# Optimization experiments

Hardware: AMD Instinct MI355X
Metric: run time of the kernel (lower is better)

## Reference

```python
import jax, jax.numpy as jnp
import numpy as np

D_HEAD = 128


def setup_inputs() -> dict:
    key = jax.random.key(0)
    k1, k2, k3 = jax.random.split(key, 3)
    batch, num_q, seq_len, d = 16, 64, 4096, D_HEAD
    query = jax.random.normal(k1, (batch, num_q, d), dtype=jnp.float32)
    keys = jax.random.normal(k2, (batch, seq_len, d), dtype=jnp.float32)
    values = jax.random.normal(k3, (batch, seq_len, d), dtype=jnp.float32)
    return {"query": query, "keys": keys, "values": values}


def reference(query, keys, values):
    # AttentionJacobian.forward with 3D query -> compute_attention_jacobian_batched
    # J[b,q] = scale * ( sum_n a[b,q,n] v[b,n] k[b,n]^T  -  (a V)[b,q] ((a K)[b,q])^T )
    d_k = keys.shape[-1]
    scale = d_k ** (-0.5)
    scores = jnp.einsum('bqd,bnd->bqn', query, keys) * scale
    attn_weights = jax.nn.softmax(scores, axis=-1)            # (b, q, n)
    attn_outputs = jnp.einsum('bqn,bnv->bqv', attn_weights, values)
    # term1 without materializing (b, q, n, v, k): fuse as single contraction
    term1 = jnp.einsum('bqn,bnv,bnk->bqvk', attn_weights, values, keys)
    weighted_keys_sum = jnp.einsum('bqn,bnk->bqk', attn_weights, keys)
    term2 = jnp.einsum('bqv,bqk->bqvk', attn_outputs, weighted_keys_sum)
    jacobians = scale * (term1 - term2)                       # (b, q, d_v, d_k)
    return jacobians
```

## Files before the change

### kernel.cpp

```cpp
#include <hip/hip_runtime.h>
#include <stdint.h>

typedef _Float16 f16;
typedef _Float16 half8 __attribute__((ext_vector_type(8)));
typedef float f32x4 __attribute__((ext_vector_type(4)));

#define BATCH 16
#define NQ 64
#define SL 4096
#define DH 128


__global__ __launch_bounds__(256) void kprep(const float* __restrict__ Kg,
                                             const float* __restrict__ Vg,
                                             f16* __restrict__ Kt,
                                             f16* __restrict__ Vt) {
  __shared__ f16 Ld[128][130];
  const int blk = blockIdx.x;
  const int b = blk >> 6;
  const int tensor = (blk >> 5) & 1;
  const int chunk = blk & 31;
  const float* src = tensor ? Vg : Kg;
  f16* dst = tensor ? Vt : Kt;
  const int t = threadIdx.x;
  const int n0 = chunk * 128;
  {
    const int d = t & 127;
    const int nl = t >> 7;
    const float* s = src + ((size_t)b * SL + n0 + nl) * DH + d;
    for (int it = 0; it < 64; ++it)
      Ld[d][nl + it * 2] = (f16)s[(size_t)it * 2 * DH];
  }
  __syncthreads();
  {
    const int r = t & 15;
    const int kc = (t >> 4) & 3;
    const int w = t >> 6;
    char* dstb = (char*)(dst + (size_t)b * DH * SL);
#pragma unroll
    for (int tl = 0; tl < 4; ++tl)
#pragma unroll
      for (int hh = 0; hh < 2; ++hh) {
        const int dhi = w + hh * 4;
        const int d = dhi * 16 + r;
        const int nl = tl * 32 + kc * 8;
        const half8 v = *(const half8*)&Ld[d][nl];
        *(half8*)(dstb + (size_t)(chunk * 4 + tl) * 8192 + dhi * 1024 +
                  kc * 256 + r * 16) = v;
      }
  }
}

__global__ __launch_bounds__(256) void kscore(const float* __restrict__ Q,
                                              const f16* __restrict__ Kt,
                                              f16* __restrict__ E) {
  const int blk = (blockIdx.x & 7) * 64 + (blockIdx.x >> 3);
  __shared__ float Qs[8][128];
  const int b = blk >> 5;
  const int qg = (blk >> 2) & 7;
  const int ns = blk & 3;
  const int t = threadIdx.x;
  for (int i = t; i < 8 * 128; i += 256)
    Qs[i >> 7][i & 127] = Q[((size_t)b * NQ + qg * 8 + (i >> 7)) * DH + (i & 127)];
  __syncthreads();
  const int w = t >> 6, l = t & 63;
  const int q0 = (w >> 1) * 4;
  const int nbase = ns * 1024 + (w & 1) * 512 + l * 8;
  const f16* kb = Kt + (size_t)b * DH * SL + (size_t)(nbase >> 5) * 4096 +
                  (size_t)((nbase >> 3) & 3) * 128;
  float acc[4][8] = {};
  for (int d = 0; d < DH; ++d) {
    const half8 kv = *(const half8*)(kb + (d >> 4) * 512 + (d & 15) * 8);
    float kf[8];
#pragma unroll
    for (int j = 0; j < 8; ++j) kf[j] = (float)kv[j];
#pragma unroll
    for (int qi = 0; qi < 4; ++qi) {
      const float qv = Qs[q0 + qi][d];
#pragma unroll
      for (int j = 0; j < 8; ++j) acc[qi][j] += qv * kf[j];
    }
  }
  const float scl = 0.08838834764831845f;
#pragma unroll
  for (int qi = 0; qi < 4; ++qi) {
    half8 ev;
#pragma unroll
    for (int j = 0; j < 8; ++j) ev[j] = (f16)__expf(acc[qi][j] * scl);
    *(half8*)&E[((size_t)b * NQ + qg * 8 + q0 + qi) * SL + nbase] = ev;
  }
}

__global__ __launch_bounds__(256) void kreduce(const f16* __restrict__ E,
                                               float* __restrict__ denom) {
  const int gw = blockIdx.x * 4 + (threadIdx.x >> 6);
  const int lane = threadIdx.x & 63;
  const f16* e = E + (size_t)gw * SL;
  float s = 0.f;
#pragma unroll
  for (int i = 0; i < 8; ++i) {
    const half8 h = *(const half8*)(e + i * 512 + lane * 8);
#pragma unroll
    for (int j = 0; j < 8; ++j) s += (float)h[j];
  }
  for (int off = 1; off < 64; off <<= 1) s += __shfl_xor(s, off);
  if (lane == 0) denom[gw] = s;
}

__global__ __launch_bounds__(256) void kev(const f16* __restrict__ Vt,
                                           const f16* __restrict__ Kt,
                                           const f16* __restrict__ E,
                                           float* __restrict__ EVp,
                                           float* __restrict__ EKp) {
  const int blk = (blockIdx.x & 7) * 32 + (blockIdx.x >> 3);
  const int b = blk >> 4;
  const int tensor = (blk >> 3) & 1;
  const int qq = (blk >> 1) & 3;
  const int nh = blk & 1;
  const char* src = (const char*)((tensor ? Kt : Vt) + (size_t)b * DH * SL);
  float* dst = (tensor ? EKp : EVp) +
               ((size_t)nh * BATCH * NQ + (size_t)b * NQ + qq * 16) * DH;
  const f16* Eb = E + ((size_t)b * NQ + qq * 16) * SL;
  const int t = threadIdx.x, w = t >> 6, l = t & 63;
  f32x4 acc[2] = {};
  for (int n0 = nh * 2048; n0 < nh * 2048 + 2048; n0 += 32) {
    const half8 a0 =
        *(const half8*)(src + (size_t)(n0 >> 5) * 8192 + w * 1024 + l * 16);
    const half8 a1 =
        *(const half8*)(src + (size_t)(n0 >> 5) * 8192 + (w + 4) * 1024 + l * 16);
    const half8 b0 =
        *(const half8*)(Eb + (size_t)(l & 15) * SL + n0 + (l >> 4) * 8);
    acc[0] = __builtin_amdgcn_mfma_f32_16x16x32_f16(a0, b0, acc[0], 0, 0, 0);
    acc[1] = __builtin_amdgcn_mfma_f32_16x16x32_f16(a1, b0, acc[1], 0, 0, 0);
  }
#pragma unroll
  for (int sv2 = 0; sv2 < 2; ++sv2) {
    const int q = l & 15;
    const int row = (w + sv2 * 4) * 16 + (l >> 4) * 4;
    *(f32x4*)&dst[(size_t)q * DH + row] = acc[sv2];
  }
}

__global__ __launch_bounds__(256, 2) void kjac(
    const f16* __restrict__ Vt, const f16* __restrict__ Kt,
    const f16* __restrict__ E, const float* __restrict__ EV,
    const float* __restrict__ EK, const float* __restrict__ denom,
    float* __restrict__ out) {
  const int blk = (blockIdx.x & 7) * 64 + (blockIdx.x >> 3);
  const int b = blk >> 5;
  const int q0 = (blk & 31) * 2;
  const int t = threadIdx.x, w = t >> 6, l = t & 63;
  const int sA = (w >> 1) * 4;
  const int sB = (w & 1) * 4;
  const char* vtb = (const char*)(Vt + (size_t)b * DH * SL) + sA * 1024 + l * 16;
  const char* ktb = (const char*)(Kt + (size_t)b * DH * SL) + sB * 1024 + l * 16;
  const f16* Eb = E + ((size_t)b * NQ + q0) * SL + (l >> 4) * 8;

  f32x4 acc[2][4][4] = {};
  half8 vfA[4], kfA[4], efA[2], vfB[4], kfB[4], efB[2];

#define LOADF(vf, kf, ef, tile)                                              \
  {                                                                          \
    const size_t gb = (size_t)(tile) * 8192;                                 \
    _Pragma("unroll") for (int i = 0; i < 4; ++i) vf[i] =                    \
        *(const half8*)(vtb + gb + i * 1024);                                \
    _Pragma("unroll") for (int j = 0; j < 4; ++j) kf[j] =                    \
        *(const half8*)(ktb + gb + j * 1024);                                \
    ef[0] = *(const half8*)(Eb + (tile) * 32);                               \
    ef[1] = *(const half8*)(Eb + SL + (tile) * 32);                          \
  }

#define MFMA32(vf, kf, ef)                                                   \
  {                                                                          \
    __builtin_amdgcn_s_setprio(1);                                           \
    _Pragma("unroll") for (int i = 0; i < 4; ++i) {                          \
      const half8 u0 = ef[0] * vf[i];                                        \
      const half8 u1 = ef[1] * vf[i];                                        \
      _Pragma("unroll") for (int j = 0; j < 4; ++j) {                        \
        acc[0][i][j] = __builtin_amdgcn_mfma_f32_16x16x32_f16(               \
            u0, kf[j], acc[0][i][j], 0, 0, 0);                               \
        acc[1][i][j] = __builtin_amdgcn_mfma_f32_16x16x32_f16(               \
            u1, kf[j], acc[1][i][j], 0, 0, 0);                               \
      }                                                                      \
    }                                                                        \
    __builtin_amdgcn_s_setprio(0);                                           \
  }

  LOADF(vfA, kfA, efA, 0)
  for (int tt = 0; tt < 126; tt += 2) {
    LOADF(vfB, kfB, efB, tt + 1)
    MFMA32(vfA, kfA, efA)
    LOADF(vfA, kfA, efA, tt + 2)
    MFMA32(vfB, kfB, efB)
  }
  LOADF(vfB, kfB, efB, 127)
  MFMA32(vfA, kfA, efA)
  MFMA32(vfB, kfB, efB)
#undef LOADF
#undef MFMA32

  const float scl = 0.08838834764831845f;
#pragma unroll
  for (int q = 0; q < 2; ++q) {
    const float invd = 1.0f / denom[b * NQ + q0 + q];
    const float* evq = EV + ((size_t)b * NQ + q0 + q) * DH;
    const float* evq2 = evq + (size_t)BATCH * NQ * DH;
    const float* ekq = EK + ((size_t)b * NQ + q0 + q) * DH;
    const float* ekq2 = ekq + (size_t)BATCH * NQ * DH;
    float* ob = out + (size_t)(b * NQ + q0 + q) * DH * DH;
#pragma unroll
    for (int i = 0; i < 4; ++i) {
      const int row0 = (sA + i) * 16 + (l >> 4) * 4;
      const f32x4 ev4 = *(const f32x4*)&evq[row0] + *(const f32x4*)&evq2[row0];
#pragma unroll
      for (int j = 0; j < 4; ++j) {
        const int col = (sB + j) * 16 + (l & 15);
        const float ek = ekq[col] + ekq2[col];
#pragma unroll
        for (int r = 0; r < 4; ++r)
          ob[(size_t)(row0 + r) * DH + col] =
              scl * invd * (acc[q][i][j][r] - invd * ev4[r] * ek);
      }
    }
  }
}

extern "C" void kernel_launch(void* const* d_in, const int* in_sizes, int n_in,
                              void* d_out, int out_size, void* d_ws,
                              size_t ws_size, hipStream_t stream) {
  const float* Q = (const float*)d_in[0];
  const float* K = (const float*)d_in[1];
  const float* V = (const float*)d_in[2];
  float* out = (float*)d_out;

  f16* Vt = (f16*)d_ws;
  f16* Kt = Vt + (size_t)BATCH * DH * SL;
  f16* Ef = Kt + (size_t)BATCH * DH * SL;
  float* EV = (float*)(Ef + (size_t)BATCH * NQ * SL);
  float* EK = EV + 2 * (size_t)BATCH * NQ * DH;
  float* denom = EK + 2 * (size_t)BATCH * NQ * DH;

  kprep<<<1024, 256, 0, stream>>>(K, V, Kt, Vt);
  kscore<<<512, 256, 0, stream>>>(Q, Kt, Ef);
  kreduce<<<256, 256, 0, stream>>>(Ef, denom);
  kev<<<256, 256, 0, stream>>>(Vt, Kt, Ef, EV, EK);
  kjac<<<512, 256, 0, stream>>>(Vt, Kt, Ef, EV, EK, denom, out);
}
```

Baseline: 185.9 us.

## Switch to 32x32x16 MFMA with matching fragment-ordered K/V layout

Changes the pre-swizzled K/V fp16 layout to match 32x32x16 MFMA operand fragments and rewrites kjac and kev to use 32x32 MFMA tiles instead of 16x16. Larger MFMA tiles raise arithmetic intensity per operand load and cut the number of MFMA issues and element-wise E*V multiplies per tile. kev is restructured to 128 blocks each covering 32 queries. This adds larger accumulator register pressure, and the epilogue stores become scalar rather than vectorised.

```diff
diff --git a/kernel.cpp b/kernel.cpp
--- a/kernel.cpp
+++ b/kernel.cpp
@@ -4,6 +4,7 @@
 typedef _Float16 f16;
 typedef _Float16 half8 __attribute__((ext_vector_type(8)));
 typedef float f32x4 __attribute__((ext_vector_type(4)));
+typedef float f32x16 __attribute__((ext_vector_type(16)));
 
 #define BATCH 16
 #define NQ 64
@@ -33,21 +34,17 @@
   }
   __syncthreads();
   {
-    const int r = t & 15;
-    const int kc = (t >> 4) & 3;
-    const int w = t >> 6;
-    char* dstb = (char*)(dst + (size_t)b * DH * SL);
-#pragma unroll
-    for (int tl = 0; tl < 4; ++tl)
-#pragma unroll
-      for (int hh = 0; hh < 2; ++hh) {
-        const int dhi = w + hh * 4;
-        const int d = dhi * 16 + r;
-        const int nl = tl * 32 + kc * 8;
-        const half8 v = *(const half8*)&Ld[d][nl];
-        *(half8*)(dstb + (size_t)(chunk * 4 + tl) * 8192 + dhi * 1024 +
-                  kc * 256 + r * 16) = v;
-      }
+    const int dblk = t >> 6;
+    const int khalf = (t >> 5) & 1;
+    const int r5 = t & 31;
+    const int d = dblk * 32 + r5;
+    f16* db = dst + (size_t)b * DH * SL;
+#pragma unroll
+    for (int ngl = 0; ngl < 8; ++ngl) {
+      const int nl = ngl * 16 + khalf * 8;
+      *(half8*)(db + (size_t)(chunk * 8 + ngl) * 2048 + dblk * 512 +
+                khalf * 256 + r5 * 8) = *(const half8*)&Ld[d][nl];
+    }
   }
 }
 
@@ -66,11 +63,11 @@
   const int w = t >> 6, l = t & 63;
   const int q0 = (w >> 1) * 4;
   const int nbase = ns * 1024 + (w & 1) * 512 + l * 8;
-  const f16* kb = Kt + (size_t)b * DH * SL + (size_t)(nbase >> 5) * 4096 +
-                  (size_t)((nbase >> 3) & 3) * 128;
+  const f16* kb = Kt + (size_t)b * DH * SL + (size_t)(nbase >> 4) * 2048 +
+                  (size_t)((nbase >> 3) & 1) * 256;
   float acc[4][8] = {};
   for (int d = 0; d < DH; ++d) {
-    const half8 kv = *(const half8*)(kb + (d >> 4) * 512 + (d & 15) * 8);
+    const half8 kv = *(const half8*)(kb + (d >> 5) * 512 + (d & 31) * 8);
     float kf[8];
 #pragma unroll
     for (int j = 0; j < 8; ++j) kf[j] = (float)kv[j];
@@ -112,32 +109,27 @@
                                            const f16* __restrict__ E,
                                            float* __restrict__ EVp,
                                            float* __restrict__ EKp) {
-  const int blk = (blockIdx.x & 7) * 32 + (blockIdx.x >> 3);
-  const int b = blk >> 4;
-  const int tensor = (blk >> 3) & 1;
-  const int qq = (blk >> 1) & 3;
-  const int nh = blk & 1;
+  const int blk = (blockIdx.x & 7) * 16 + (blockIdx.x >> 3);
+  const int b = blk >> 3;
+  const int tensor = (blk >> 2) & 1;
+  const int nh = (blk >> 1) & 1;
+  const int qh = blk & 1;
   const char* src = (const char*)((tensor ? Kt : Vt) + (size_t)b * DH * SL);
-  float* dst = (tensor ? EKp : EVp) +
-               ((size_t)nh * BATCH * NQ + (size_t)b * NQ + qq * 16) * DH;
-  const f16* Eb = E + ((size_t)b * NQ + qq * 16) * SL;
+  float* dst = (tensor ? EKp : EVp) + ((size_t)nh * BATCH * NQ + (size_t)b * NQ) * DH;
+  const f16* Eb = E + ((size_t)b * NQ + qh * 32) * SL;
   const int t = threadIdx.x, w = t >> 6, l = t & 63;
-  f32x4 acc[2] = {};
-  for (int n0 = nh * 2048; n0 < nh * 2048 + 2048; n0 += 32) {
-    const half8 a0 =
-        *(const half8*)(src + (size_t)(n0 >> 5) * 8192 + w * 1024 + l * 16);
-    const half8 a1 =
-        *(const half8*)(src + (size_t)(n0 >> 5) * 8192 + (w + 4) * 1024 + l * 16);
-    const half8 b0 =
-        *(const half8*)(Eb + (size_t)(l & 15) * SL + n0 + (l >> 4) * 8);
-    acc[0] = __builtin_amdgcn_mfma_f32_16x16x32_f16(a0, b0, acc[0], 0, 0, 0);
-    acc[1] = __builtin_amdgcn_mfma_f32_16x16x32_f16(a1, b0, acc[1], 0, 0, 0);
-  }
-#pragma unroll
-  for (int sv2 = 0; sv2 < 2; ++sv2) {
-    const int q = l & 15;
-    const int row = (w + sv2 * 4) * 16 + (l >> 4) * 4;
-    *(f32x4*)&dst[(size_t)q * DH + row] = acc[sv2];
+  f32x16 acc = {};
+  for (int ng = nh * 128; ng < nh * 128 + 128; ++ng) {
+    const half8 a = *(const half8*)(src + (size_t)ng * 4096 + w * 1024 + l * 16);
+    const half8 bb =
+        *(const half8*)(Eb + (size_t)(l & 31) * SL + ng * 16 + (l >> 5) * 8);
+    acc = __builtin_amdgcn_mfma_f32_32x32x16_f16(a, bb, acc, 0, 0, 0);
+  }
+  const int q = qh * 32 + (l & 31);
+#pragma unroll
+  for (int reg = 0; reg < 16; ++reg) {
+    const int row = w * 32 + (reg & 3) + 8 * (reg >> 2) + 4 * (l >> 5);
+    dst[(size_t)q * DH + row] = acc[reg];
   }
 }
 
@@ -150,37 +142,44 @@
   const int b = blk >> 5;
   const int q0 = (blk & 31) * 2;
   const int t = threadIdx.x, w = t >> 6, l = t & 63;
-  const int sA = (w >> 1) * 4;
-  const int sB = (w & 1) * 4;
-  const char* vtb = (const char*)(Vt + (size_t)b * DH * SL) + sA * 1024 + l * 16;
-  const char* ktb = (const char*)(Kt + (size_t)b * DH * SL) + sB * 1024 + l * 16;
-  const f16* Eb = E + ((size_t)b * NQ + q0) * SL + (l >> 4) * 8;
-
-  f32x4 acc[2][4][4] = {};
-  half8 vfA[4], kfA[4], efA[2], vfB[4], kfB[4], efB[2];
+  const int Mb = (w >> 1) * 64;
+  const int Nb = (w & 1) * 64;
+  const char* vtb =
+      (const char*)(Vt + (size_t)b * DH * SL) + (Mb >> 5) * 1024 + l * 16;
+  const char* ktb =
+      (const char*)(Kt + (size_t)b * DH * SL) + (Nb >> 5) * 1024 + l * 16;
+  const f16* Eb = E + ((size_t)b * NQ + q0) * SL + (l >> 5) * 8;
+
+  f32x16 acc[2][2][2] = {};
+  half8 vfA[2][2], kfA[2][2], efA[2][2];
+  half8 vfB[2][2], kfB[2][2], efB[2][2];
 
 #define LOADF(vf, kf, ef, tile)                                              \
   {                                                                          \
     const size_t gb = (size_t)(tile) * 8192;                                 \
-    _Pragma("unroll") for (int i = 0; i < 4; ++i) vf[i] =                    \
-        *(const half8*)(vtb + gb + i * 1024);                                \
-    _Pragma("unroll") for (int j = 0; j < 4; ++j) kf[j] =                    \
-        *(const half8*)(ktb + gb + j * 1024);                                \
-    ef[0] = *(const half8*)(Eb + (tile) * 32);                               \
-    ef[1] = *(const half8*)(Eb + SL + (tile) * 32);                          \
-  }
-
-#define MFMA32(vf, kf, ef)                                                   \
+    _Pragma("unroll") for (int s = 0; s < 2; ++s) {                          \
+      _Pragma("unroll") for (int di = 0; di < 2; ++di) vf[di][s] =           \
+          *(const half8*)(vtb + gb + s * 4096 + di * 1024);                  \
+      _Pragma("unroll") for (int dj = 0; dj < 2; ++dj) kf[dj][s] =           \
+          *(const half8*)(ktb + gb + s * 4096 + dj * 1024);                  \
+      _Pragma("unroll") for (int q = 0; q < 2; ++q) ef[q][s] =               \
+          *(const half8*)(Eb + q * SL + (tile) * 32 + s * 16);               \
+    }                                                                        \
+  }
+
+#define MFMA16(vf, kf, ef)                                                   \
   {                                                                          \
     __builtin_amdgcn_s_setprio(1);                                           \
-    _Pragma("unroll") for (int i = 0; i < 4; ++i) {                          \
-      const half8 u0 = ef[0] * vf[i];                                        \
-      const half8 u1 = ef[1] * vf[i];                                        \
-      _Pragma("unroll") for (int j = 0; j < 4; ++j) {                        \
-        acc[0][i][j] = __builtin_amdgcn_mfma_f32_16x16x32_f16(               \
-            u0, kf[j], acc[0][i][j], 0, 0, 0);                               \
-        acc[1][i][j] = __builtin_amdgcn_mfma_f32_16x16x32_f16(               \
-            u1, kf[j], acc[1][i][j], 0, 0, 0);                               \
+    _Pragma("unroll") for (int q = 0; q < 2; ++q) {                          \
+      _Pragma("unroll") for (int di = 0; di < 2; ++di) {                     \
+        const half8 u0 = ef[q][0] * vf[di][0];                               \
+        const half8 u1 = ef[q][1] * vf[di][1];                               \
+        _Pragma("unroll") for (int dj = 0; dj < 2; ++dj) {                   \
+          acc[q][di][dj] = __builtin_amdgcn_mfma_f32_32x32x16_f16(           \
+              u0, kf[dj][0], acc[q][di][dj], 0, 0, 0);                       \
+          acc[q][di][dj] = __builtin_amdgcn_mfma_f32_32x32x16_f16(           \
+              u1, kf[dj][1], acc[q][di][dj], 0, 0, 0);                       \
+        }                                                                    \
       }                                                                      \
     }                                                                        \
     __builtin_amdgcn_s_setprio(0);                                           \
@@ -189,15 +188,15 @@
   LOADF(vfA, kfA, efA, 0)
   for (int tt = 0; tt < 126; tt += 2) {
     LOADF(vfB, kfB, efB, tt + 1)
-    MFMA32(vfA, kfA, efA)
+    MFMA16(vfA, kfA, efA)
     LOADF(vfA, kfA, efA, tt + 2)
-    MFMA32(vfB, kfB, efB)
+    MFMA16(vfB, kfB, efB)
   }
   LOADF(vfB, kfB, efB, 127)
-  MFMA32(vfA, kfA, efA)
-  MFMA32(vfB, kfB, efB)
+  MFMA16(vfA, kfA, efA)
+  MFMA16(vfB, kfB, efB)
 #undef LOADF
-#undef MFMA32
+#undef MFMA16
 
   const float scl = 0.08838834764831845f;
 #pragma unroll
@@ -209,17 +208,21 @@
     const float* ekq2 = ekq + (size_t)BATCH * NQ * DH;
     float* ob = out + (size_t)(b * NQ + q0 + q) * DH * DH;
 #pragma unroll
-    for (int i = 0; i < 4; ++i) {
-      const int row0 = (sA + i) * 16 + (l >> 4) * 4;
-      const f32x4 ev4 = *(const f32x4*)&evq[row0] + *(const f32x4*)&evq2[row0];
-#pragma unroll
-      for (int j = 0; j < 4; ++j) {
-        const int col = (sB + j) * 16 + (l & 15);
+    for (int di = 0; di < 2; ++di) {
+#pragma unroll
+      for (int dj = 0; dj < 2; ++dj) {
+        const int col = Nb + dj * 32 + (l & 31);
         const float ek = ekq[col] + ekq2[col];
 #pragma unroll
-        for (int r = 0; r < 4; ++r)
-          ob[(size_t)(row0 + r) * DH + col] =
-              scl * invd * (acc[q][i][j][r] - invd * ev4[r] * ek);
+        for (int rg = 0; rg < 4; ++rg) {
+          const int row0 = Mb + di * 32 + rg * 8 + 4 * (l >> 5);
+          const f32x4 ev4 =
+              *(const f32x4*)&evq[row0] + *(const f32x4*)&evq2[row0];
+#pragma unroll
+          for (int rr = 0; rr < 4; ++rr)
+            ob[(size_t)(row0 + rr) * DH + col] =
+                scl * invd * (acc[q][di][dj][rg * 4 + rr] - invd * ev4[rr] * ek);
+        }
       }
     }
   }
@@ -243,6 +246,6 @@
   kprep<<<1024, 256, 0, stream>>>(K, V, Kt, Vt);
   kscore<<<512, 256, 0, stream>>>(Q, Kt, Ef);
   kreduce<<<256, 256, 0, stream>>>(Ef, denom);
-  kev<<<256, 256, 0, stream>>>(Vt, Kt, Ef, EV, EK);
+  kev<<<128, 256, 0, stream>>>(Vt, Kt, Ef, EV, EK);
   kjac<<<512, 256, 0, stream>>>(Vt, Kt, Ef, EV, EK, denom, out);
 }
```

Measured after the change: 231.0 us. 24.2% more time.

## Fuse softmax denominator reduction into kev and restage E through LDS

Applied to the files above, without the earlier changes.

Removes the separate kreduce kernel. The V-tensor blocks of kev now compute partial row sums of E while loading it. kev is reorganized so each block handles 32 queries over a quarter of the sequence, staging E tiles in shared memory and reusing each K/V fragment across two query subtiles. kjac sums four partials for EV, EK and the denominator. This trades one launch and one full read of E for extra syncthreads per chunk and more partial-sum reads in the epilogue.

```diff
diff --git a/kernel.cpp b/kernel.cpp
--- a/kernel.cpp
+++ b/kernel.cpp
@@ -2,6 +2,7 @@
 #include <stdint.h>
 
 typedef _Float16 f16;
+typedef _Float16 half4 __attribute__((ext_vector_type(4)));
 typedef _Float16 half8 __attribute__((ext_vector_type(8)));
 typedef float f32x4 __attribute__((ext_vector_type(4)));
 
@@ -91,60 +92,74 @@
   }
 }
 
-__global__ __launch_bounds__(256) void kreduce(const f16* __restrict__ E,
-                                               float* __restrict__ denom) {
-  const int gw = blockIdx.x * 4 + (threadIdx.x >> 6);
-  const int lane = threadIdx.x & 63;
-  const f16* e = E + (size_t)gw * SL;
-  float s = 0.f;
-#pragma unroll
-  for (int i = 0; i < 8; ++i) {
-    const half8 h = *(const half8*)(e + i * 512 + lane * 8);
-#pragma unroll
-    for (int j = 0; j < 8; ++j) s += (float)h[j];
-  }
-  for (int off = 1; off < 64; off <<= 1) s += __shfl_xor(s, off);
-  if (lane == 0) denom[gw] = s;
-}
-
 __global__ __launch_bounds__(256) void kev(const f16* __restrict__ Vt,
                                            const f16* __restrict__ Kt,
                                            const f16* __restrict__ E,
                                            float* __restrict__ EVp,
-                                           float* __restrict__ EKp) {
+                                           float* __restrict__ EKp,
+                                           float* __restrict__ denomp) {
+  __shared__ __align__(16) f16 Es[32][40];
   const int blk = (blockIdx.x & 7) * 32 + (blockIdx.x >> 3);
   const int b = blk >> 4;
   const int tensor = (blk >> 3) & 1;
-  const int qq = (blk >> 1) & 3;
-  const int nh = blk & 1;
+  const int nq = (blk >> 1) & 3;
+  const int qh = blk & 1;
   const char* src = (const char*)((tensor ? Kt : Vt) + (size_t)b * DH * SL);
   float* dst = (tensor ? EKp : EVp) +
-               ((size_t)nh * BATCH * NQ + (size_t)b * NQ + qq * 16) * DH;
-  const f16* Eb = E + ((size_t)b * NQ + qq * 16) * SL;
+               ((size_t)nq * BATCH * NQ + (size_t)b * NQ + qh * 32) * DH;
+  const f16* Eb = E + ((size_t)b * NQ + qh * 32) * SL + nq * 1024;
   const int t = threadIdx.x, w = t >> 6, l = t & 63;
-  f32x4 acc[2] = {};
-  for (int n0 = nh * 2048; n0 < nh * 2048 + 2048; n0 += 32) {
-    const half8 a0 =
-        *(const half8*)(src + (size_t)(n0 >> 5) * 8192 + w * 1024 + l * 16);
-    const half8 a1 =
-        *(const half8*)(src + (size_t)(n0 >> 5) * 8192 + (w + 4) * 1024 + l * 16);
-    const half8 b0 =
-        *(const half8*)(Eb + (size_t)(l & 15) * SL + n0 + (l >> 4) * 8);
-    acc[0] = __builtin_amdgcn_mfma_f32_16x16x32_f16(a0, b0, acc[0], 0, 0, 0);
-    acc[1] = __builtin_amdgcn_mfma_f32_16x16x32_f16(a1, b0, acc[1], 0, 0, 0);
-  }
-#pragma unroll
-  for (int sv2 = 0; sv2 < 2; ++sv2) {
-    const int q = l & 15;
-    const int row = (w + sv2 * 4) * 16 + (l >> 4) * 4;
-    *(f32x4*)&dst[(size_t)q * DH + row] = acc[sv2];
+  const int eq = t >> 3;
+  const int en = (t & 7) * 4;
+
+  f32x4 acc[2][2] = {};
+  float dsum = 0.f;
+
+  for (int chunk = 0; chunk < 32; ++chunk) {
+    const half4 ev4 = *(const half4*)(Eb + (size_t)eq * SL + chunk * 32 + en);
+    *(half4*)&Es[eq][en] = ev4;
+    if (!tensor)
+      dsum += (float)ev4[0] + (float)ev4[1] + (float)ev4[2] + (float)ev4[3];
+    __syncthreads();
+    const int n0 = nq * 1024 + chunk * 32;
+    const size_t gb = (size_t)(n0 >> 5) * 8192 + l * 16;
+    const half8 a0 = *(const half8*)(src + gb + w * 1024);
+    const half8 a1 = *(const half8*)(src + gb + (w + 4) * 1024);
+    half8 b0, b1;
+#pragma unroll
+    for (int j = 0; j < 8; ++j) {
+      b0[j] = Es[l & 15][(l >> 4) * 8 + j];
+      b1[j] = Es[16 + (l & 15)][(l >> 4) * 8 + j];
+    }
+    acc[0][0] = __builtin_amdgcn_mfma_f32_16x16x32_f16(a0, b0, acc[0][0], 0, 0, 0);
+    acc[0][1] = __builtin_amdgcn_mfma_f32_16x16x32_f16(a0, b1, acc[0][1], 0, 0, 0);
+    acc[1][0] = __builtin_amdgcn_mfma_f32_16x16x32_f16(a1, b0, acc[1][0], 0, 0, 0);
+    acc[1][1] = __builtin_amdgcn_mfma_f32_16x16x32_f16(a1, b1, acc[1][1], 0, 0, 0);
+    __syncthreads();
+  }
+
+#pragma unroll
+  for (int sv2 = 0; sv2 < 2; ++sv2)
+#pragma unroll
+    for (int qsub = 0; qsub < 2; ++qsub) {
+      const int q = qsub * 16 + (l & 15);
+      const int row = (w + sv2 * 4) * 16 + (l >> 4) * 4;
+      *(f32x4*)&dst[(size_t)q * DH + row] = acc[sv2][qsub];
+    }
+
+  if (!tensor) {
+    dsum += __shfl_xor(dsum, 1);
+    dsum += __shfl_xor(dsum, 2);
+    dsum += __shfl_xor(dsum, 4);
+    if ((t & 7) == 0)
+      denomp[(size_t)nq * BATCH * NQ + (size_t)b * NQ + qh * 32 + eq] = dsum;
   }
 }
 
 __global__ __launch_bounds__(256, 2) void kjac(
     const f16* __restrict__ Vt, const f16* __restrict__ Kt,
     const f16* __restrict__ E, const float* __restrict__ EV,
-    const float* __restrict__ EK, const float* __restrict__ denom,
+    const float* __restrict__ EK, const float* __restrict__ denomp,
     float* __restrict__ out) {
   const int blk = (blockIdx.x & 7) * 64 + (blockIdx.x >> 3);
   const int b = blk >> 5;
@@ -200,22 +215,30 @@
 #undef MFMA32
 
   const float scl = 0.08838834764831845f;
+  const size_t PS = (size_t)BATCH * NQ * DH;
+  const size_t DS = (size_t)BATCH * NQ;
 #pragma unroll
   for (int q = 0; q < 2; ++q) {
-    const float invd = 1.0f / denom[b * NQ + q0 + q];
-    const float* evq = EV + ((size_t)b * NQ + q0 + q) * DH;
-    const float* evq2 = evq + (size_t)BATCH * NQ * DH;
-    const float* ekq = EK + ((size_t)b * NQ + q0 + q) * DH;
-    const float* ekq2 = ekq + (size_t)BATCH * NQ * DH;
-    float* ob = out + (size_t)(b * NQ + q0 + q) * DH * DH;
+    const size_t qi = (size_t)b * NQ + q0 + q;
+    float den = 0.f;
+#pragma unroll
+    for (int p = 0; p < 4; ++p) den += denomp[p * DS + qi];
+    const float invd = 1.0f / den;
+    const float* evq = EV + qi * DH;
+    const float* ekq = EK + qi * DH;
+    float* ob = out + qi * DH * DH;
 #pragma unroll
     for (int i = 0; i < 4; ++i) {
       const int row0 = (sA + i) * 16 + (l >> 4) * 4;
-      const f32x4 ev4 = *(const f32x4*)&evq[row0] + *(const f32x4*)&evq2[row0];
+      f32x4 ev4 = *(const f32x4*)&evq[row0];
+#pragma unroll
+      for (int p = 1; p < 4; ++p) ev4 += *(const f32x4*)&evq[p * PS + row0];
 #pragma unroll
       for (int j = 0; j < 4; ++j) {
         const int col = (sB + j) * 16 + (l & 15);
-        const float ek = ekq[col] + ekq2[col];
+        float ek = ekq[col];
+#pragma unroll
+        for (int p = 1; p < 4; ++p) ek += ekq[p * PS + col];
 #pragma unroll
         for (int r = 0; r < 4; ++r)
           ob[(size_t)(row0 + r) * DH + col] =
@@ -236,13 +259,12 @@
   f16* Vt = (f16*)d_ws;
   f16* Kt = Vt + (size_t)BATCH * DH * SL;
   f16* Ef = Kt + (size_t)BATCH * DH * SL;
-  float* EV = (float*)(Ef + (size_t)BATCH * NQ * SL);
-  float* EK = EV + 2 * (size_t)BATCH * NQ * DH;
-  float* denom = EK + 2 * (size_t)BATCH * NQ * DH;
+  float* EVp = (float*)(Ef + (size_t)BATCH * NQ * SL);
+  float* EKp = EVp + 4 * (size_t)BATCH * NQ * DH;
+  float* denomp = EKp + 4 * (size_t)BATCH * NQ * DH;
 
   kprep<<<1024, 256, 0, stream>>>(K, V, Kt, Vt);
   kscore<<<512, 256, 0, stream>>>(Q, Kt, Ef);
-  kreduce<<<256, 256, 0, stream>>>(Ef, denom);
-  kev<<<256, 256, 0, stream>>>(Vt, Kt, Ef, EV, EK);
-  kjac<<<512, 256, 0, stream>>>(Vt, Kt, Ef, EV, EK, denom, out);
-}
+  kev<<<256, 256, 0, stream>>>(Vt, Kt, Ef, EVp, EKp, denomp);
+  kjac<<<512, 256, 0, stream>>>(Vt, Kt, Ef, EVp, EKp, denomp, out);
+}
```

Result: faster. 181.7 us (-2.3%).
